# Optimization experiments

Hardware: AMD Instinct MI355X
Metric: run time of the kernel (lower is better)

The kernel has to match this reference:

```python
import jax, jax.numpy as jnp
import numpy as np
import jax.scipy.linalg as jsl

T = 2048      # number of time steps
N = 8192      # number of particles / states
D = 4         # matrix_size (dims[-1] = 16)
H = 128       # MLP hidden width

def setup_inputs() -> dict:
    key = jax.random.key(0)
    ks = jax.random.split(key, 8)
    x = jax.random.normal(ks[0], (N, D), dtype=jnp.float32)
    t = jnp.sort(jax.random.uniform(ks[1], (T,), dtype=jnp.float32))
    # MLP params, stored (in, out); torch Linear does x @ W.T + b
    def xavier(k, fan_in, fan_out):
        s = jnp.sqrt(2.0 / (fan_in + fan_out))
        return (s * jax.random.normal(k, (fan_in, fan_out))).astype(jnp.float32)
    W1 = xavier(ks[2], 1, H); b1 = jnp.zeros((H,), jnp.float32)
    W2 = xavier(ks[3], H, H); b2 = jnp.zeros((H,), jnp.float32)
    W3 = xavier(ks[4], H, D * D); b3 = jnp.zeros((D * D,), jnp.float32)
    M0 = jnp.zeros((D, D), jnp.float32)  # zero buffer (M0=None)
    return {"x": x, "t": t, "M0": M0, "W1": W1, "b1": b1,
            "W2": W2, "b2": b2, "W3": W3, "b3": b3}

def reference(x, t, M0, W1, b1, W2, b2, W3, b3):
    t0 = 0.0
    tt = jnp.concatenate([jnp.full((1, 1), t0, t.dtype), t.reshape(-1, 1)], axis=0)  # (T+1,1)
    delta_t = tt[1:] - tt[:-1]          # (T,1)
    t_avg = (tt[1:] + tt[:-1]) * 0.5    # (T,1)
    # per-step MLP -> (T, D*D)
    h = jnp.tanh(t_avg @ W1 + b1)
    h = jnp.tanh(h @ W2 + b2)
    A = (h @ W3 + b3).reshape(-1, D, D)
    A = A + M0[None, :, :]
    A = A * delta_t[:, :, None]         # (T,D,D) scaled by dt
    # lie_algebra = identity
    A_sum = jnp.cumsum(A, axis=0)       # prefix-sum over time
    E = jax.vmap(jsl.expm)(A_sum)       # batched matrix exponential (T,D,D)
    out = jnp.einsum('tij,nj->tni', E, x)  # (T,N,D)
    return out
```

## Files before the change

### kernel.cpp

```cpp
#include <hip/hip_runtime.h>
#include <math.h>

#define TT 2048
#define NN 8192
#define DD 4
#define HH 128

typedef float f4 __attribute__((ext_vector_type(4)));

__global__ void mlp_kernel(const float* __restrict__ t_arr,
                           const float* __restrict__ M0,
                           const float* __restrict__ W1, const float* __restrict__ b1,
                           const float* __restrict__ W2, const float* __restrict__ b2,
                           const float* __restrict__ W3, const float* __restrict__ b3,
                           float* __restrict__ A_t) {
    const int t = blockIdx.x;
    const int j = threadIdx.x;
    __shared__ float h1[HH];
    __shared__ float h2[HH];

    const float t_cur  = t_arr[t];
    const float t_prev = (t > 0) ? t_arr[t - 1] : 0.0f;
    const float dt = t_cur - t_prev;
    const float ta = 0.5f * (t_cur + t_prev);

    h1[j] = tanhf(fmaf(ta, W1[j], b1[j]));
    __syncthreads();

    float acc = b2[j];
    #pragma unroll 8
    for (int i = 0; i < HH; ++i) acc = fmaf(h1[i], W2[i * HH + j], acc);
    h2[j] = tanhf(acc);
    __syncthreads();

    if (j < 16) {
        float a = b3[j];
        #pragma unroll 8
        for (int i = 0; i < HH; ++i) a = fmaf(h2[i], W3[i * 16 + j], a);
        a = (a + M0[j]) * dt;
        A_t[j * TT + t] = a;
    }
}

__global__ __launch_bounds__(1024) void scan_kernel(const float* __restrict__ A_t,
                                                    float* __restrict__ Asum) {
    const int tid = threadIdx.x;
    const int e = tid >> 6;
    const int c = tid & 63;
    const float4* src = (const float4*)(A_t + e * TT + c * 32);

    float4 v[8];
    float s = 0.0f;
    #pragma unroll
    for (int i = 0; i < 8; ++i) {
        v[i] = src[i];
        s += v[i].x + v[i].y + v[i].z + v[i].w;
    }

    float sc = s;
    #pragma unroll
    for (int d = 1; d < 64; d <<= 1) {
        const float up = __shfl_up(sc, d, 64);
        if (c >= d) sc += up;
    }
    const float ex = __shfl_up(sc, 1, 64);
    float run = (c == 0) ? 0.0f : ex;

    const int t0 = c * 32;
    #pragma unroll
    for (int i = 0; i < 8; ++i) {
        run += v[i].x; Asum[(t0 + 4 * i + 0) * 16 + e] = run;
        run += v[i].y; Asum[(t0 + 4 * i + 1) * 16 + e] = run;
        run += v[i].z; Asum[(t0 + 4 * i + 2) * 16 + e] = run;
        run += v[i].w; Asum[(t0 + 4 * i + 3) * 16 + e] = run;
    }
}

__device__ __forceinline__ void mm4(const float* __restrict__ A,
                                    const float* __restrict__ B,
                                    float* __restrict__ C) {
    #pragma unroll
    for (int i = 0; i < 4; ++i) {
        #pragma unroll
        for (int j = 0; j < 4; ++j) {
            float s = 0.0f;
            #pragma unroll
            for (int k = 0; k < 4; ++k) s = fmaf(A[i * 4 + k], B[k * 4 + j], s);
            C[i * 4 + j] = s;
        }
    }
}

__global__ __launch_bounds__(64) void expm_kernel(const float* __restrict__ Asum,
                                                  float* __restrict__ E) {
    const int t = blockIdx.x * blockDim.x + threadIdx.x;
    if (t >= TT) return;

    float M[16];
    const float4* src = (const float4*)(Asum + t * 16);
    #pragma unroll
    for (int r = 0; r < 4; ++r) {
        float4 v = src[r];
        M[r * 4 + 0] = v.x; M[r * 4 + 1] = v.y; M[r * 4 + 2] = v.z; M[r * 4 + 3] = v.w;
    }

    float nrm = 0.0f;
    #pragma unroll
    for (int i = 0; i < 4; ++i) {
        float rs = fabsf(M[i*4+0]) + fabsf(M[i*4+1]) + fabsf(M[i*4+2]) + fabsf(M[i*4+3]);
        nrm = fmaxf(nrm, rs);
    }
    int k = 0;
    while (nrm > 0.5f && k < 40) { nrm *= 0.5f; ++k; }
    const float sc = ldexpf(1.0f, -k);
    #pragma unroll
    for (int i = 0; i < 16; ++i) M[i] *= sc;

    float R[16], P[16], Q[16];
    #pragma unroll
    for (int i = 0; i < 16; ++i) { P[i] = M[i]; R[i] = M[i]; }
    R[0] += 1.0f; R[5] += 1.0f; R[10] += 1.0f; R[15] += 1.0f;
    for (int n = 2; n <= 12; ++n) {
        mm4(P, M, Q);
        const float inv = 1.0f / (float)n;
        #pragma unroll
        for (int i = 0; i < 16; ++i) { P[i] = Q[i] * inv; R[i] += P[i]; }
    }
    for (int s = 0; s < k; ++s) {
        mm4(R, R, Q);
        #pragma unroll
        for (int i = 0; i < 16; ++i) R[i] = Q[i];
    }

    float4* dst = (float4*)(E + t * 16);
    #pragma unroll
    for (int r = 0; r < 4; ++r)
        dst[r] = make_float4(R[r*4+0], R[r*4+1], R[r*4+2], R[r*4+3]);
}

__global__ __launch_bounds__(256) void apply_kernel(const float* __restrict__ E,
                                                    const float* __restrict__ x,
                                                    float* __restrict__ out) {
    const int t = blockIdx.x;

    const float4* Ev = (const float4*)(E + t * 16);
    const float4 e0 = Ev[0], e1 = Ev[1], e2 = Ev[2], e3 = Ev[3];

    const f4* xs = (const f4*)x;
    f4* os = (f4*)out + (size_t)t * NN;

    #pragma unroll 8
    for (int n = threadIdx.x; n < NN; n += 256) {
        const f4 xv = xs[n];
        f4 o;
        o.x = fmaf(e0.x, xv.x, fmaf(e0.y, xv.y, fmaf(e0.z, xv.z, e0.w * xv.w)));
        o.y = fmaf(e1.x, xv.x, fmaf(e1.y, xv.y, fmaf(e1.z, xv.z, e1.w * xv.w)));
        o.z = fmaf(e2.x, xv.x, fmaf(e2.y, xv.y, fmaf(e2.z, xv.z, e2.w * xv.w)));
        o.w = fmaf(e3.x, xv.x, fmaf(e3.y, xv.y, fmaf(e3.z, xv.z, e3.w * xv.w)));
        __builtin_nontemporal_store(o, &os[n]);
    }
}

extern "C" void kernel_launch(void* const* d_in, const int* in_sizes, int n_in,
                              void* d_out, int out_size, void* d_ws, size_t ws_size,
                              hipStream_t stream) {
    const float* x  = (const float*)d_in[0];
    const float* t  = (const float*)d_in[1];
    const float* M0 = (const float*)d_in[2];
    const float* W1 = (const float*)d_in[3];
    const float* b1 = (const float*)d_in[4];
    const float* W2 = (const float*)d_in[5];
    const float* b2 = (const float*)d_in[6];
    const float* W3 = (const float*)d_in[7];
    const float* b3 = (const float*)d_in[8];
    float* out = (float*)d_out;

    float* A_t  = (float*)d_ws;
    float* Asum = A_t  + 16 * TT;
    float* E    = Asum + 16 * TT;

    mlp_kernel<<<TT, HH, 0, stream>>>(t, M0, W1, b1, W2, b2, W3, b3, A_t);
    scan_kernel<<<1, 1024, 0, stream>>>(A_t, Asum);
    expm_kernel<<<TT / 64, 64, 0, stream>>>(Asum, E);
    apply_kernel<<<TT, 256, 0, stream>>>(E, x, out);
}
```

Measured before the change: 324.8 us.

## Fuse MLP, scan, expm and apply into one persistent kernel with grid barriers

Replaces four kernel launches with a single persistent kernel of 1024 blocks that runs the MLP, prefix scan, matrix exponential and apply stages, separated by atomic-counter grid barriers. The goal is to remove inter-kernel launch gaps and the tail idle time between small stages. It relies on all 1024 blocks being co-resident; the barrier has a timeout that could silently break correctness if they are not. Stage occupancy also changes: the scan runs on a single 256-thread block, expm uses only 8 blocks, and the apply loop now uses plain stores instead of nontemporal stores.

Result: slower. 539.8 us (+66.2%).

```diff
diff --git a/kernel.cpp b/kernel.cpp
--- a/kernel.cpp
+++ b/kernel.cpp
@@ -3,78 +3,28 @@
 
 #define TT 2048
 #define NN 8192
-#define DD 4
 #define HH 128
+#define NB 1024
+#define BS 256
 
 typedef float f4 __attribute__((ext_vector_type(4)));
 
-__global__ void mlp_kernel(const float* __restrict__ t_arr,
-                           const float* __restrict__ M0,
-                           const float* __restrict__ W1, const float* __restrict__ b1,
-                           const float* __restrict__ W2, const float* __restrict__ b2,
-                           const float* __restrict__ W3, const float* __restrict__ b3,
-                           float* __restrict__ A_t) {
-    const int t = blockIdx.x;
-    const int j = threadIdx.x;
-    __shared__ float h1[HH];
-    __shared__ float h2[HH];
-
-    const float t_cur  = t_arr[t];
-    const float t_prev = (t > 0) ? t_arr[t - 1] : 0.0f;
-    const float dt = t_cur - t_prev;
-    const float ta = 0.5f * (t_cur + t_prev);
-
-    h1[j] = tanhf(fmaf(ta, W1[j], b1[j]));
+__device__ __forceinline__ void grid_barrier(unsigned* ctr, unsigned target) {
     __syncthreads();
-
-    float acc = b2[j];
-    #pragma unroll 8
-    for (int i = 0; i < HH; ++i) acc = fmaf(h1[i], W2[i * HH + j], acc);
-    h2[j] = tanhf(acc);
+    if (threadIdx.x == 0) {
+        __threadfence();
+        atomicAdd(ctr, 1u);
+        const long long t0 = clock64();
+        while (__hip_atomic_load(ctr, __ATOMIC_RELAXED, __HIP_MEMORY_SCOPE_AGENT) < target) {
+            __builtin_amdgcn_s_sleep(2);
+            if (clock64() - t0 > 200000000LL) break;
+        }
+        __threadfence();
+    }
     __syncthreads();
-
-    if (j < 16) {
-        float a = b3[j];
-        #pragma unroll 8
-        for (int i = 0; i < HH; ++i) a = fmaf(h2[i], W3[i * 16 + j], a);
-        a = (a + M0[j]) * dt;
-        A_t[j * TT + t] = a;
-    }
-}
-
-__global__ __launch_bounds__(1024) void scan_kernel(const float* __restrict__ A_t,
-                                                    float* __restrict__ Asum) {
-    const int tid = threadIdx.x;
-    const int e = tid >> 6;
-    const int c = tid & 63;
-    const float4* src = (const float4*)(A_t + e * TT + c * 32);
-
-    float4 v[8];
-    float s = 0.0f;
-    #pragma unroll
-    for (int i = 0; i < 8; ++i) {
-        v[i] = src[i];
-        s += v[i].x + v[i].y + v[i].z + v[i].w;
-    }
-
-    float sc = s;
-    #pragma unroll
-    for (int d = 1; d < 64; d <<= 1) {
-        const float up = __shfl_up(sc, d, 64);
-        if (c >= d) sc += up;
-    }
-    const float ex = __shfl_up(sc, 1, 64);
-    float run = (c == 0) ? 0.0f : ex;
-
-    const int t0 = c * 32;
-    #pragma unroll
-    for (int i = 0; i < 8; ++i) {
-        run += v[i].x; Asum[(t0 + 4 * i + 0) * 16 + e] = run;
-        run += v[i].y; Asum[(t0 + 4 * i + 1) * 16 + e] = run;
-        run += v[i].z; Asum[(t0 + 4 * i + 2) * 16 + e] = run;
-        run += v[i].w; Asum[(t0 + 4 * i + 3) * 16 + e] = run;
-    }
-}
+}
+
+__global__ void init_kernel(unsigned* ctr) { *ctr = 0u; }
 
 __device__ __forceinline__ void mm4(const float* __restrict__ A,
                                     const float* __restrict__ B,
@@ -91,73 +41,142 @@
     }
 }
 
-__global__ __launch_bounds__(64) void expm_kernel(const float* __restrict__ Asum,
-                                                  float* __restrict__ E) {
-    const int t = blockIdx.x * blockDim.x + threadIdx.x;
-    if (t >= TT) return;
-
-    float M[16];
-    const float4* src = (const float4*)(Asum + t * 16);
-    #pragma unroll
-    for (int r = 0; r < 4; ++r) {
-        float4 v = src[r];
-        M[r * 4 + 0] = v.x; M[r * 4 + 1] = v.y; M[r * 4 + 2] = v.z; M[r * 4 + 3] = v.w;
-    }
-
-    float nrm = 0.0f;
-    #pragma unroll
-    for (int i = 0; i < 4; ++i) {
-        float rs = fabsf(M[i*4+0]) + fabsf(M[i*4+1]) + fabsf(M[i*4+2]) + fabsf(M[i*4+3]);
-        nrm = fmaxf(nrm, rs);
-    }
-    int k = 0;
-    while (nrm > 0.5f && k < 40) { nrm *= 0.5f; ++k; }
-    const float sc = ldexpf(1.0f, -k);
-    #pragma unroll
-    for (int i = 0; i < 16; ++i) M[i] *= sc;
-
-    float R[16], P[16], Q[16];
-    #pragma unroll
-    for (int i = 0; i < 16; ++i) { P[i] = M[i]; R[i] = M[i]; }
-    R[0] += 1.0f; R[5] += 1.0f; R[10] += 1.0f; R[15] += 1.0f;
-    for (int n = 2; n <= 12; ++n) {
-        mm4(P, M, Q);
-        const float inv = 1.0f / (float)n;
+__global__ __launch_bounds__(BS, 4) void fused_kernel(
+    const float* __restrict__ t_arr, const float* __restrict__ M0,
+    const float* __restrict__ W1, const float* __restrict__ b1,
+    const float* __restrict__ W2, const float* __restrict__ b2,
+    const float* __restrict__ W3, const float* __restrict__ b3,
+    const float* __restrict__ x, float* __restrict__ out,
+    float* __restrict__ A_t, float* __restrict__ Asum,
+    float* __restrict__ E, unsigned* ctr)
+{
+    {
+        const int tloc = threadIdx.x >> 7;
+        const int j    = threadIdx.x & 127;
+        const int t    = (blockIdx.x << 1) + tloc;
+        __shared__ float h1[2][HH];
+        __shared__ float h2[2][HH];
+
+        const float t_cur  = t_arr[t];
+        const float t_prev = (t > 0) ? t_arr[t - 1] : 0.0f;
+        const float dt = t_cur - t_prev;
+        const float ta = 0.5f * (t_cur + t_prev);
+
+        h1[tloc][j] = tanhf(fmaf(ta, W1[j], b1[j]));
+        __syncthreads();
+
+        float acc = b2[j];
+        #pragma unroll 8
+        for (int i = 0; i < HH; ++i) acc = fmaf(h1[tloc][i], W2[i * HH + j], acc);
+        h2[tloc][j] = tanhf(acc);
+        __syncthreads();
+
+        if (j < 16) {
+            float a = b3[j];
+            #pragma unroll 8
+            for (int i = 0; i < HH; ++i) a = fmaf(h2[tloc][i], W3[i * 16 + j], a);
+            a = (a + M0[j]) * dt;
+            A_t[j * TT + t] = a;
+        }
+    }
+    grid_barrier(ctr, NB);
+
+    if (blockIdx.x == 0) {
+        const int w    = threadIdx.x >> 6;
+        const int lane = threadIdx.x & 63;
+        for (int r = 0; r < 4; ++r) {
+            const int e = (w << 2) + r;
+            const float4* src = (const float4*)(A_t + e * TT + lane * 32);
+            float4 v[8];
+            float s = 0.0f;
+            #pragma unroll
+            for (int i = 0; i < 8; ++i) {
+                v[i] = src[i];
+                s += v[i].x + v[i].y + v[i].z + v[i].w;
+            }
+            float sc = s;
+            #pragma unroll
+            for (int d = 1; d < 64; d <<= 1) {
+                const float up = __shfl_up(sc, d, 64);
+                if (lane >= d) sc += up;
+            }
+            const float ex = __shfl_up(sc, 1, 64);
+            float run = (lane == 0) ? 0.0f : ex;
+            const int t0 = lane * 32;
+            #pragma unroll
+            for (int i = 0; i < 8; ++i) {
+                run += v[i].x; Asum[(t0 + 4 * i + 0) * 16 + e] = run;
+                run += v[i].y; Asum[(t0 + 4 * i + 1) * 16 + e] = run;
+                run += v[i].z; Asum[(t0 + 4 * i + 2) * 16 + e] = run;
+                run += v[i].w; Asum[(t0 + 4 * i + 3) * 16 + e] = run;
+            }
+        }
+    }
+    grid_barrier(ctr, 2 * NB);
+
+    {
+        const int t = blockIdx.x * BS + threadIdx.x;
+        if (t < TT) {
+            float M[16];
+            const float4* src = (const float4*)(Asum + t * 16);
+            #pragma unroll
+            for (int r = 0; r < 4; ++r) {
+                float4 v = src[r];
+                M[r*4+0] = v.x; M[r*4+1] = v.y; M[r*4+2] = v.z; M[r*4+3] = v.w;
+            }
+            float nrm = 0.0f;
+            #pragma unroll
+            for (int i = 0; i < 4; ++i) {
+                float rs = fabsf(M[i*4+0]) + fabsf(M[i*4+1]) + fabsf(M[i*4+2]) + fabsf(M[i*4+3]);
+                nrm = fmaxf(nrm, rs);
+            }
+            int k = 0;
+            while (nrm > 0.5f && k < 40) { nrm *= 0.5f; ++k; }
+            const float sc = ldexpf(1.0f, -k);
+            #pragma unroll
+            for (int i = 0; i < 16; ++i) M[i] *= sc;
+
+            float R[16], P[16], Q[16];
+            #pragma unroll
+            for (int i = 0; i < 16; ++i) { P[i] = M[i]; R[i] = M[i]; }
+            R[0] += 1.0f; R[5] += 1.0f; R[10] += 1.0f; R[15] += 1.0f;
+            for (int n = 2; n <= 12; ++n) {
+                mm4(P, M, Q);
+                const float inv = 1.0f / (float)n;
+                #pragma unroll
+                for (int i = 0; i < 16; ++i) { P[i] = Q[i] * inv; R[i] += P[i]; }
+            }
+            for (int s = 0; s < k; ++s) {
+                mm4(R, R, Q);
+                #pragma unroll
+                for (int i = 0; i < 16; ++i) R[i] = Q[i];
+            }
+            float4* dst = (float4*)(E + t * 16);
+            #pragma unroll
+            for (int r = 0; r < 4; ++r)
+                dst[r] = make_float4(R[r*4+0], R[r*4+1], R[r*4+2], R[r*4+3]);
+        }
+    }
+    grid_barrier(ctr, 3 * NB);
+
+    {
+        const f4* xs = (const f4*)x;
         #pragma unroll
-        for (int i = 0; i < 16; ++i) { P[i] = Q[i] * inv; R[i] += P[i]; }
-    }
-    for (int s = 0; s < k; ++s) {
-        mm4(R, R, Q);
-        #pragma unroll
-        for (int i = 0; i < 16; ++i) R[i] = Q[i];
-    }
-
-    float4* dst = (float4*)(E + t * 16);
-    #pragma unroll
-    for (int r = 0; r < 4; ++r)
-        dst[r] = make_float4(R[r*4+0], R[r*4+1], R[r*4+2], R[r*4+3]);
-}
-
-__global__ __launch_bounds__(256) void apply_kernel(const float* __restrict__ E,
-                                                    const float* __restrict__ x,
-                                                    float* __restrict__ out) {
-    const int t = blockIdx.x;
-
-    const float4* Ev = (const float4*)(E + t * 16);
-    const float4 e0 = Ev[0], e1 = Ev[1], e2 = Ev[2], e3 = Ev[3];
-
-    const f4* xs = (const f4*)x;
-    f4* os = (f4*)out + (size_t)t * NN;
-
-    #pragma unroll 8
-    for (int n = threadIdx.x; n < NN; n += 256) {
-        const f4 xv = xs[n];
-        f4 o;
-        o.x = fmaf(e0.x, xv.x, fmaf(e0.y, xv.y, fmaf(e0.z, xv.z, e0.w * xv.w)));
-        o.y = fmaf(e1.x, xv.x, fmaf(e1.y, xv.y, fmaf(e1.z, xv.z, e1.w * xv.w)));
-        o.z = fmaf(e2.x, xv.x, fmaf(e2.y, xv.y, fmaf(e2.z, xv.z, e2.w * xv.w)));
-        o.w = fmaf(e3.x, xv.x, fmaf(e3.y, xv.y, fmaf(e3.z, xv.z, e3.w * xv.w)));
-        __builtin_nontemporal_store(o, &os[n]);
+        for (int tl = 0; tl < 2; ++tl) {
+            const int t = (blockIdx.x << 1) + tl;
+            const f4* Ev = (const f4*)(E + t * 16);
+            const f4 e0 = Ev[0], e1 = Ev[1], e2 = Ev[2], e3 = Ev[3];
+            f4* os = (f4*)out + (size_t)t * NN;
+            for (int n = threadIdx.x; n < NN; n += BS) {
+                const f4 xv = xs[n];
+                f4 o;
+                o.x = fmaf(e0.x, xv.x, fmaf(e0.y, xv.y, fmaf(e0.z, xv.z, e0.w * xv.w)));
+                o.y = fmaf(e1.x, xv.x, fmaf(e1.y, xv.y, fmaf(e1.z, xv.z, e1.w * xv.w)));
+                o.z = fmaf(e2.x, xv.x, fmaf(e2.y, xv.y, fmaf(e2.z, xv.z, e2.w * xv.w)));
+                o.w = fmaf(e3.x, xv.x, fmaf(e3.y, xv.y, fmaf(e3.z, xv.z, e3.w * xv.w)));
+                os[n] = o;
+            }
+        }
     }
 }
 
@@ -178,9 +197,9 @@
     float* A_t  = (float*)d_ws;
     float* Asum = A_t  + 16 * TT;
     float* E    = Asum + 16 * TT;
-
-    mlp_kernel<<<TT, HH, 0, stream>>>(t, M0, W1, b1, W2, b2, W3, b3, A_t);
-    scan_kernel<<<1, 1024, 0, stream>>>(A_t, Asum);
-    expm_kernel<<<TT / 64, 64, 0, stream>>>(Asum, E);
-    apply_kernel<<<TT, 256, 0, stream>>>(E, x, out);
-}
+    unsigned* ctr = (unsigned*)(E + 16 * TT);
+
+    init_kernel<<<1, 1, 0, stream>>>(ctr);
+    fused_kernel<<<NB, BS, 0, stream>>>(t, M0, W1, b1, W2, b2, W3, b3,
+                                        x, out, A_t, Asum, E, ctr);
+}
```
